# Optimization experiments

Hardware: AMD Instinct MI355X
Metric: run time of the kernel (lower is better)

Reference implementation:

```python
import jax, jax.numpy as jnp
import numpy as np

NUM_HEADS = 16  # matches init_kwargs


def _linear(x, W, b):
    # torch nn.Linear: x @ W.T + b
    return jnp.matmul(x, W.T) + b


def setup_inputs() -> dict:
    key = jax.random.key(0)
    ks = jax.random.split(key, 5)
    B, S, Dm = 8, 2048, 1024
    scale = 0.02
    return {
        "q": jax.random.normal(ks[0], (B, S, Dm), dtype=jnp.float32),
        "k": jax.random.normal(ks[1], (B, S, Dm), dtype=jnp.float32),
        "v": jax.random.normal(ks[2], (B, S, Dm), dtype=jnp.float32),
        "W": jax.random.normal(ks[3], (Dm, Dm), dtype=jnp.float32) * scale,
        "b": jax.random.normal(ks[4], (Dm,), dtype=jnp.float32) * scale,
    }


def reference(q, k, v, W, b):
    B, S, Dm = q.shape
    H = NUM_HEADS
    D = Dm // H  # head_dim

    def proj(x):
        # linear -> view(B, S, H, D) -> transpose(2, 3): (B, S, D, H)
        # NOTE: original code transposes dims 2 and 3 (head_dim <-> heads),
        # NOT the usual (1, 2); we reproduce that exactly.
        y = _linear(x, W, b).reshape(B, S, H, D)
        return jnp.swapaxes(y, 2, 3)  # (B, S, D, H)

    qh, kh, vh = proj(q), proj(k), proj(v)

    # scores: (B, S, D, H) @ (B, S, H, D) -> (B, S, D, D), scaled by sqrt(head_dim)
    logits = jnp.einsum("bsdh,bseh->bsde", qh, kh) / jnp.sqrt(jnp.float32(D))
    attn = jax.nn.softmax(logits, axis=-1)
    out = jnp.einsum("bsde,bseh->bsdh", attn, vh)  # (B, S, D, H)

    # transpose(1, 2) -> (B, D, S, H), then view(B, -1, model_dim)
    concat = jnp.swapaxes(out, 1, 2).reshape(B, -1, Dm)  # (B, S, Dm)
    return _linear(concat, W, b)
```

## Files before the change

kernel.cpp:

```cpp
#include <hip/hip_runtime.h>
#include <hip/hip_fp16.h>
#include <math.h>

typedef _Float16 f16;
typedef _Float16 half8_t __attribute__((ext_vector_type(8)));
typedef _Float16 half4_t __attribute__((ext_vector_type(4)));
typedef _Float16 half2_t __attribute__((ext_vector_type(2)));
typedef __fp16   fp16x2  __attribute__((ext_vector_type(2)));
typedef float    float4_t __attribute__((ext_vector_type(4)));

__device__ f16 Wh[1024 * 1024];
__device__ f16 Xh[3ul * 16777216];

__device__ __forceinline__ void gl_lds16(const void* g, void* l) {
    __builtin_amdgcn_global_load_lds(
        (const __attribute__((address_space(1))) void*)g,
        (__attribute__((address_space(3))) void*)l,
        16, 0, 0);
}

__device__ __forceinline__ half2_t pkrtz(float a, float b) {
    fp16x2 r = __builtin_amdgcn_cvt_pkrtz(a, b);
    return __builtin_bit_cast(half2_t, r);
}

__device__ __forceinline__ half8_t cvt8(float4_t lo, float4_t hi) {
    half2_t p0 = pkrtz(lo[0], lo[1]);
    half2_t p1 = pkrtz(lo[2], lo[3]);
    half2_t p2 = pkrtz(hi[0], hi[1]);
    half2_t p3 = pkrtz(hi[2], hi[3]);
    half8_t r;
    r[0] = p0[0]; r[1] = p0[1]; r[2] = p1[0]; r[3] = p1[1];
    r[4] = p2[0]; r[5] = p2[1]; r[6] = p3[0]; r[7] = p3[1];
    return r;
}

__global__ __launch_bounds__(256) void convert_w_kernel(const float* __restrict__ W) {
    const int i = (blockIdx.x * 256 + threadIdx.x) * 8;
    const float4_t a = *(const float4_t*)(W + i);
    const float4_t b = *(const float4_t*)(W + i + 4);
    half8_t h;
#pragma unroll
    for (int t = 0; t < 4; ++t) h[t] = (f16)a[t];
#pragma unroll
    for (int t = 0; t < 4; ++t) h[4 + t] = (f16)b[t];
    *(half8_t*)(Wh + i) = h;
}

__global__ __launch_bounds__(256) void convert_x_kernel(
    const float* __restrict__ q, const float* __restrict__ k,
    const float* __restrict__ v)
{
    const int z = blockIdx.z;
    const float* src = (z == 0) ? q : (z == 1) ? k : v;
    f16* dst = Xh + (size_t)z * 16777216;
    const size_t i = ((size_t)blockIdx.x * 256 + threadIdx.x) * 8;
    const float4_t a = *(const float4_t*)(src + i);
    const float4_t b = *(const float4_t*)(src + i + 4);
    *(half8_t*)(dst + i) = cvt8(a, b);
}


__device__ __forceinline__ void stage16(const f16* __restrict__ base, f16* dst,
                                        int tid, int kt) {
#pragma unroll
    for (int it = 0; it < 4; ++it) {
        const int ch = tid + it * 512;
        const int r = ch >> 3, s = ch & 7;
        gl_lds16(base + (size_t)r * 1024 + kt + ((s ^ (r & 7)) << 3), dst + ch * 8);
    }
}

template <typename TC>
__device__ __forceinline__ void gemm_tile256(const f16* __restrict__ A,
                                             const float* __restrict__ bias,
                                             TC* __restrict__ C,
                                             int row0, int col0) {
    constexpr int K = 1024, N = 1024, NT = 16;
    __shared__ __align__(16) f16 smem[65536];
    f16* const Asb = smem;
    f16* const Bsb = smem + 32768;

    const int tid  = threadIdx.x;
    const int lane = tid & 63;
    const int wave = tid >> 6;
    const int wr   = wave >> 2;
    const int wc   = wave & 3;
    const int lrow = lane & 15;
    const int kq   = lane >> 4;

    const f16* const Ag = A + (size_t)row0 * K;
    const f16* const Bg = Wh + (size_t)col0 * K;

    float4_t acc[8][4];
#pragma unroll
    for (int i = 0; i < 8; ++i)
#pragma unroll
        for (int j = 0; j < 4; ++j)
            acc[i][j] = (float4_t){0.f, 0.f, 0.f, 0.f};

    stage16(Ag, Asb, tid, 0);
    stage16(Bg, Bsb, tid, 0);

    for (int u = 0; u < NT; ++u) {
        const int cur = u & 1;
        const f16* const Ac = Asb + (cur << 14);
        const f16* const Bc = Bsb + (cur << 14);
        f16* const An = Asb + ((cur ^ 1) << 14);
        f16* const Bn = Bsb + ((cur ^ 1) << 14);
        const int kn = ((u + 1) & (NT - 1)) * 64;

        stage16(Ag, An, tid, kn);
        stage16(Bg, Bn, tid, kn);
        asm volatile("s_waitcnt vmcnt(8)" ::: "memory");
        __builtin_amdgcn_s_barrier();

        half8_t bfv[4][2];
#pragma unroll
        for (int j = 0; j < 4; ++j) {
            const int n = wc * 64 + j * 16 + lrow;
#pragma unroll
            for (int ks = 0; ks < 2; ++ks)
                bfv[j][ks] = *(const half8_t*)(Bc + n * 64 + (((ks * 4 + kq) ^ (n & 7)) << 3));
        }

        {
            half8_t afv[4][2];
#pragma unroll
            for (int i = 0; i < 4; ++i) {
                const int m = wr * 128 + i * 16 + lrow;
#pragma unroll
                for (int ks = 0; ks < 2; ++ks)
                    afv[i][ks] = *(const half8_t*)(Ac + m * 64 + (((ks * 4 + kq) ^ (m & 7)) << 3));
            }
            __builtin_amdgcn_s_setprio(1);
#pragma unroll
            for (int i = 0; i < 4; ++i)
#pragma unroll
                for (int j = 0; j < 4; ++j)
#pragma unroll
                    for (int ks = 0; ks < 2; ++ks)
                        acc[i][j] = __builtin_amdgcn_mfma_f32_16x16x32_f16(
                            afv[i][ks], bfv[j][ks], acc[i][j], 0, 0, 0);
            __builtin_amdgcn_s_setprio(0);
        }

        {
            half8_t afv[4][2];
#pragma unroll
            for (int i = 0; i < 4; ++i) {
                const int m = wr * 128 + (4 + i) * 16 + lrow;
#pragma unroll
                for (int ks = 0; ks < 2; ++ks)
                    afv[i][ks] = *(const half8_t*)(Ac + m * 64 + (((ks * 4 + kq) ^ (m & 7)) << 3));
            }
            __builtin_amdgcn_s_setprio(1);
#pragma unroll
            for (int i = 0; i < 4; ++i)
#pragma unroll
                for (int j = 0; j < 4; ++j)
#pragma unroll
                    for (int ks = 0; ks < 2; ++ks)
                        acc[4 + i][j] = __builtin_amdgcn_mfma_f32_16x16x32_f16(
                            afv[i][ks], bfv[j][ks], acc[4 + i][j], 0, 0, 0);
            __builtin_amdgcn_s_setprio(0);
        }

        asm volatile("s_waitcnt lgkmcnt(0)" ::: "memory");
        __builtin_amdgcn_s_barrier();
    }
    asm volatile("s_waitcnt vmcnt(0)" ::: "memory");

    const int ccol  = lane & 15;
    const int rbase = (lane >> 4) << 2;
#pragma unroll
    for (int j = 0; j < 4; ++j) {
        const int gcol = col0 + wc * 64 + j * 16 + ccol;
        const float bv = bias[gcol];
#pragma unroll
        for (int i = 0; i < 8; ++i) {
#pragma unroll
            for (int r = 0; r < 4; ++r) {
                const int grow = row0 + wr * 128 + i * 16 + rbase + r;
                C[(size_t)grow * N + gcol] = (TC)(acc[i][j][r] + bv);
            }
        }
    }
}

template <typename TC>
__global__ __launch_bounds__(512, 2) void gemm_kernel(
    const f16* __restrict__ A, const float* __restrict__ bias,
    TC* __restrict__ C) {
    const int f    = blockIdx.x + 64 * blockIdx.y;
    const int virt = (f & 7) * 32 + (f >> 3);
    gemm_tile256<TC>(A, bias, C, ((virt >> 2) & 63) * 256, (virt & 3) * 256);
}

__global__ __launch_bounds__(512, 2) void gemm_proj_kernel(
    const float* __restrict__ bias,
    f16* __restrict__ cq, f16* __restrict__ ck, f16* __restrict__ cv) {
    const int f    = blockIdx.x + 64 * (blockIdx.y + 4 * blockIdx.z);
    const int virt = (f & 7) * 96 + (f >> 3);
    const int y = virt & 3, x = (virt >> 2) & 63, z = virt >> 8;
    f16* C = (z == 0) ? cq : (z == 1) ? ck : cv;
    gemm_tile256<f16>(Xh + (size_t)z * 16777216, bias, C, x * 256, y * 256);
}

__global__ __launch_bounds__(256) void attn_kernel(
    const f16* __restrict__ pq, const f16* __restrict__ pk,
    const f16* __restrict__ pv, f16* __restrict__ outp)
{
    __shared__ __align__(16) f16 Qs[4][64][24];
    __shared__ __align__(16) f16 Ks[4][64][24];
    __shared__ __align__(16) f16 Vs[4][16][72];
    __shared__ __align__(16) f16 Os[4][64][24];
    const int lane = threadIdx.x & 63;
    const int wave = threadIdx.x >> 6;
    const int p0 = blockIdx.x * 4;
    const int p = p0 + wave;
    const f16* qptr = pq + (size_t)p * 1024;
    const f16* kptr = pk + (size_t)p * 1024;
    const f16* vptr = pv + (size_t)p * 1024;

    {
        const int h  = lane >> 2;
        const int c0 = (lane & 3) << 4;
        const half8_t q0 = *(const half8_t*)(qptr + lane * 16);
        const half8_t q1 = *(const half8_t*)(qptr + lane * 16 + 8);
        const half8_t k0 = *(const half8_t*)(kptr + lane * 16);
        const half8_t k1 = *(const half8_t*)(kptr + lane * 16 + 8);
#pragma unroll
        for (int t = 0; t < 8; ++t) {
            Qs[wave][c0 + t][h]     = q0[t];
            Qs[wave][c0 + 8 + t][h] = q1[t];
            Ks[wave][c0 + t][h]     = k0[t];
            Ks[wave][c0 + 8 + t][h] = k1[t];
        }
        const half8_t v0 = *(const half8_t*)(vptr + lane * 16);
        const half8_t v1 = *(const half8_t*)(vptr + lane * 16 + 8);
        *(half8_t*)&Vs[wave][h][c0]     = v0;
        *(half8_t*)&Vs[wave][h][c0 + 8] = v1;
    }
    __syncthreads();

    const int g  = lane >> 4;
    const int lc = lane & 15;

    half4_t ka[4], qb[4];
#pragma unroll
    for (int t = 0; t < 4; ++t) {
        ka[t] = *(const half4_t*)&Ks[wave][16 * t + lc][4 * g];
        qb[t] = *(const half4_t*)&Qs[wave][16 * t + lc][4 * g];
    }
    float4_t s[4][4];
#pragma unroll
    for (int et = 0; et < 4; ++et)
#pragma unroll
        for (int dt = 0; dt < 4; ++dt)
            s[et][dt] = __builtin_amdgcn_mfma_f32_16x16x16f16(
                ka[et], qb[dt], (float4_t){0.f, 0.f, 0.f, 0.f}, 0, 0, 0);

    float inv[4];
#pragma unroll
    for (int dt = 0; dt < 4; ++dt) {
        float m = s[0][dt][0];
#pragma unroll
        for (int et = 0; et < 4; ++et)
#pragma unroll
            for (int r = 0; r < 4; ++r) m = fmaxf(m, s[et][dt][r]);
        m = fmaxf(m, __shfl_xor(m, 16));
        m = fmaxf(m, __shfl_xor(m, 32));
        float sum = 0.f;
#pragma unroll
        for (int et = 0; et < 4; ++et)
#pragma unroll
            for (int r = 0; r < 4; ++r) {
                const float t = __expf((s[et][dt][r] - m) * 0.125f);
                s[et][dt][r] = t;
                sum += t;
            }
        sum += __shfl_xor(sum, 16);
        sum += __shfl_xor(sum, 32);
        inv[dt] = 1.f / sum;
    }

    half4_t pa[4][4];
#pragma unroll
    for (int kt = 0; kt < 4; ++kt)
#pragma unroll
        for (int dt = 0; dt < 4; ++dt) {
            const half2_t lo = pkrtz(s[kt][dt][0] * inv[dt], s[kt][dt][1] * inv[dt]);
            const half2_t hi = pkrtz(s[kt][dt][2] * inv[dt], s[kt][dt][3] * inv[dt]);
            half4_t f;
            f[0] = lo[0]; f[1] = lo[1]; f[2] = hi[0]; f[3] = hi[1];
            pa[kt][dt] = f;
        }

    float4_t o[4];
#pragma unroll
    for (int dt = 0; dt < 4; ++dt) o[dt] = (float4_t){0.f, 0.f, 0.f, 0.f};
#pragma unroll
    for (int kt = 0; kt < 4; ++kt) {
        const half4_t vb = *(const half4_t*)&Vs[wave][lc][16 * kt + 4 * g];
#pragma unroll
        for (int dt = 0; dt < 4; ++dt)
            o[dt] = __builtin_amdgcn_mfma_f32_16x16x16f16(pa[kt][dt], vb, o[dt], 0, 0, 0);
    }

#pragma unroll
    for (int dt = 0; dt < 4; ++dt)
#pragma unroll
        for (int r = 0; r < 4; ++r)
            Os[wave][16 * dt + 4 * g + r][lc] = (f16)o[dt][r];
    __syncthreads();

    const int b0 = p0 >> 11;
    const int s0 = p0 & 2047;
#pragma unroll
    for (int hf = 0; hf < 2; ++hf) {
        const int u  = threadIdx.x + hf * 256;
        const int d  = u >> 3;
        const int si = (u >> 1) & 3;
        const int uh = u & 1;
        const half8_t val = *(const half8_t*)&Os[si][d][uh * 8];
        f16* dst = outp + ((size_t)(b0 * 64 + d) * 2048 + (s0 + si)) * 16 + uh * 8;
        *(half8_t*)dst = val;
    }
}

extern "C" void kernel_launch(void* const* d_in, const int* in_sizes, int n_in,
                              void* d_out, int out_size, void* d_ws, size_t ws_size,
                              hipStream_t stream)
{
    const float* q    = (const float*)d_in[0];
    const float* k    = (const float*)d_in[1];
    const float* v    = (const float*)d_in[2];
    const float* W    = (const float*)d_in[3];
    const float* bias = (const float*)d_in[4];
    float* out = (float*)d_out;

    const int M = 16384;
    const size_t elems = (size_t)M * 1024;

    f16* projq = (f16*)d_ws;
    f16* attn  = projq + elems;
    f16* projk = (f16*)d_out;
    f16* projv = projk + elems;

    convert_w_kernel<<<512, 256, 0, stream>>>(W);
    dim3 gridc(8192, 1, 3);
    convert_x_kernel<<<gridc, 256, 0, stream>>>(q, k, v);

    dim3 gridp(M / 256, 1024 / 256, 3);
    gemm_proj_kernel<<<gridp, 512, 0, stream>>>(bias, projq, projk, projv);
    attn_kernel<<<M / 4, 256, 0, stream>>>(projq, projk, projv, attn);
    dim3 gridf(M / 256, 1024 / 256);
    gemm_kernel<float><<<gridf, 512, 0, stream>>>(attn, bias, out);
}
```

Before: 446.4 us.

## Interleave half-tile prefetches with MFMA quadrants and stage fp16 epilogue through LDS

Splits each K-step of the 256x256 GEMM into four MFMA quadrants and spreads half-sized global-to-LDS loads between them. The A tile is now prefetched two steps ahead into the buffer just consumed, and the B tile one step ahead. This gives finer-grained overlap of memory loads with compute, at the cost of more barriers per iteration. For fp16 outputs, the epilogue writes results to swizzled LDS and then stores coalesced 16-byte vectors to global memory instead of scattered 2-byte stores.

```diff
diff --git a/kernel.cpp b/kernel.cpp
--- a/kernel.cpp
+++ b/kernel.cpp
@@ -61,10 +61,10 @@
 }
 
 
-__device__ __forceinline__ void stage16(const f16* __restrict__ base, f16* dst,
-                                        int tid, int kt) {
-#pragma unroll
-    for (int it = 0; it < 4; ++it) {
+__device__ __forceinline__ void stage_half(const f16* __restrict__ base, f16* dst,
+                                           int tid, int kt, int half) {
+#pragma unroll
+    for (int it = 2 * half; it < 2 * half + 2; ++it) {
         const int ch = tid + it * 512;
         const int r = ch >> 3, s = ch & 7;
         gl_lds16(base + (size_t)r * 1024 + kt + ((s ^ (r & 7)) << 3), dst + ch * 8);
@@ -99,90 +99,153 @@
         for (int j = 0; j < 4; ++j)
             acc[i][j] = (float4_t){0.f, 0.f, 0.f, 0.f};
 
-    stage16(Ag, Asb, tid, 0);
-    stage16(Bg, Bsb, tid, 0);
+    stage_half(Ag, Asb, tid, 0, 0);
+    stage_half(Ag, Asb, tid, 0, 1);
+    stage_half(Bg, Bsb, tid, 0, 0);
+    stage_half(Bg, Bsb, tid, 0, 1);
+    stage_half(Ag, Asb + 16384, tid, 64, 0);
+    stage_half(Ag, Asb + 16384, tid, 64, 1);
 
     for (int u = 0; u < NT; ++u) {
-        const int cur = u & 1;
-        const f16* const Ac = Asb + (cur << 14);
-        const f16* const Bc = Bsb + (cur << 14);
-        f16* const An = Asb + ((cur ^ 1) << 14);
-        f16* const Bn = Bsb + ((cur ^ 1) << 14);
-        const int kn = ((u + 1) & (NT - 1)) * 64;
-
-        stage16(Ag, An, tid, kn);
-        stage16(Bg, Bn, tid, kn);
-        asm volatile("s_waitcnt vmcnt(8)" ::: "memory");
-        __builtin_amdgcn_s_barrier();
-
-        half8_t bfv[4][2];
-#pragma unroll
-        for (int j = 0; j < 4; ++j) {
+        const int c = u & 1;
+        const f16* const Ac = Asb + (c << 14);
+        const f16* const Bc = Bsb + (c << 14);
+        f16* const Bn = Bsb + ((c ^ 1) << 14);
+        f16* const Af = Asb + (c << 14);
+        const int k1 = ((u + 1) & (NT - 1)) * 64;
+        const int k2 = ((u + 2) & (NT - 1)) * 64;
+
+        half8_t afv[8][2], bfv[4][2];
+
+        stage_half(Bg, Bn, tid, k1, 0);
+        asm volatile("s_waitcnt vmcnt(6)" ::: "memory");
+        __builtin_amdgcn_s_barrier();
+#pragma unroll
+        for (int i = 0; i < 4; ++i) {
+            const int m = wr * 128 + i * 16 + lrow;
+#pragma unroll
+            for (int ks = 0; ks < 2; ++ks)
+                afv[i][ks] = *(const half8_t*)(Ac + m * 64 + (((ks * 4 + kq) ^ (m & 7)) << 3));
+        }
+#pragma unroll
+        for (int j = 0; j < 2; ++j) {
             const int n = wc * 64 + j * 16 + lrow;
 #pragma unroll
             for (int ks = 0; ks < 2; ++ks)
                 bfv[j][ks] = *(const half8_t*)(Bc + n * 64 + (((ks * 4 + kq) ^ (n & 7)) << 3));
         }
-
-        {
-            half8_t afv[4][2];
-#pragma unroll
-            for (int i = 0; i < 4; ++i) {
-                const int m = wr * 128 + i * 16 + lrow;
+        __builtin_amdgcn_s_setprio(1);
+#pragma unroll
+        for (int i = 0; i < 4; ++i)
+#pragma unroll
+            for (int j = 0; j < 2; ++j)
 #pragma unroll
                 for (int ks = 0; ks < 2; ++ks)
-                    afv[i][ks] = *(const half8_t*)(Ac + m * 64 + (((ks * 4 + kq) ^ (m & 7)) << 3));
-            }
-            __builtin_amdgcn_s_setprio(1);
-#pragma unroll
-            for (int i = 0; i < 4; ++i)
-#pragma unroll
-                for (int j = 0; j < 4; ++j)
-#pragma unroll
-                    for (int ks = 0; ks < 2; ++ks)
-                        acc[i][j] = __builtin_amdgcn_mfma_f32_16x16x32_f16(
-                            afv[i][ks], bfv[j][ks], acc[i][j], 0, 0, 0);
-            __builtin_amdgcn_s_setprio(0);
-        }
-
-        {
-            half8_t afv[4][2];
-#pragma unroll
-            for (int i = 0; i < 4; ++i) {
-                const int m = wr * 128 + (4 + i) * 16 + lrow;
+                    acc[i][j] = __builtin_amdgcn_mfma_f32_16x16x32_f16(
+                        afv[i][ks], bfv[j][ks], acc[i][j], 0, 0, 0);
+        __builtin_amdgcn_s_setprio(0);
+        __builtin_amdgcn_s_barrier();
+
+#pragma unroll
+        for (int i = 4; i < 8; ++i) {
+            const int m = wr * 128 + i * 16 + lrow;
+#pragma unroll
+            for (int ks = 0; ks < 2; ++ks)
+                afv[i][ks] = *(const half8_t*)(Ac + m * 64 + (((ks * 4 + kq) ^ (m & 7)) << 3));
+        }
+#pragma unroll
+        for (int j = 2; j < 4; ++j) {
+            const int n = wc * 64 + j * 16 + lrow;
+#pragma unroll
+            for (int ks = 0; ks < 2; ++ks)
+                bfv[j][ks] = *(const half8_t*)(Bc + n * 64 + (((ks * 4 + kq) ^ (n & 7)) << 3));
+        }
+        stage_half(Bg, Bn, tid, k1, 1);
+        __builtin_amdgcn_s_barrier();
+        __builtin_amdgcn_s_setprio(1);
+#pragma unroll
+        for (int i = 0; i < 4; ++i)
+#pragma unroll
+            for (int j = 2; j < 4; ++j)
 #pragma unroll
                 for (int ks = 0; ks < 2; ++ks)
-                    afv[i][ks] = *(const half8_t*)(Ac + m * 64 + (((ks * 4 + kq) ^ (m & 7)) << 3));
-            }
-            __builtin_amdgcn_s_setprio(1);
-#pragma unroll
-            for (int i = 0; i < 4; ++i)
-#pragma unroll
-                for (int j = 0; j < 4; ++j)
-#pragma unroll
-                    for (int ks = 0; ks < 2; ++ks)
-                        acc[4 + i][j] = __builtin_amdgcn_mfma_f32_16x16x32_f16(
-                            afv[i][ks], bfv[j][ks], acc[4 + i][j], 0, 0, 0);
-            __builtin_amdgcn_s_setprio(0);
-        }
-
+                    acc[i][j] = __builtin_amdgcn_mfma_f32_16x16x32_f16(
+                        afv[i][ks], bfv[j][ks], acc[i][j], 0, 0, 0);
+        __builtin_amdgcn_s_setprio(0);
         asm volatile("s_waitcnt lgkmcnt(0)" ::: "memory");
         __builtin_amdgcn_s_barrier();
+
+        stage_half(Ag, Af, tid, k2, 0);
+        __builtin_amdgcn_s_barrier();
+        __builtin_amdgcn_s_setprio(1);
+#pragma unroll
+        for (int i = 4; i < 8; ++i)
+#pragma unroll
+            for (int j = 0; j < 2; ++j)
+#pragma unroll
+                for (int ks = 0; ks < 2; ++ks)
+                    acc[i][j] = __builtin_amdgcn_mfma_f32_16x16x32_f16(
+                        afv[i][ks], bfv[j][ks], acc[i][j], 0, 0, 0);
+        __builtin_amdgcn_s_setprio(0);
+        __builtin_amdgcn_s_barrier();
+
+        stage_half(Ag, Af, tid, k2, 1);
+        __builtin_amdgcn_s_barrier();
+        __builtin_amdgcn_s_setprio(1);
+#pragma unroll
+        for (int i = 4; i < 8; ++i)
+#pragma unroll
+            for (int j = 2; j < 4; ++j)
+#pragma unroll
+                for (int ks = 0; ks < 2; ++ks)
+                    acc[i][j] = __builtin_amdgcn_mfma_f32_16x16x32_f16(
+                        afv[i][ks], bfv[j][ks], acc[i][j], 0, 0, 0);
+        __builtin_amdgcn_s_setprio(0);
+        __builtin_amdgcn_s_barrier();
     }
     asm volatile("s_waitcnt vmcnt(0)" ::: "memory");
+    __builtin_amdgcn_s_barrier();
 
     const int ccol  = lane & 15;
     const int rbase = (lane >> 4) << 2;
-#pragma unroll
-    for (int j = 0; j < 4; ++j) {
-        const int gcol = col0 + wc * 64 + j * 16 + ccol;
-        const float bv = bias[gcol];
-#pragma unroll
-        for (int i = 0; i < 8; ++i) {
-#pragma unroll
-            for (int r = 0; r < 4; ++r) {
-                const int grow = row0 + wr * 128 + i * 16 + rbase + r;
-                C[(size_t)grow * N + gcol] = (TC)(acc[i][j][r] + bv);
+
+    if constexpr (sizeof(TC) == 2) {
+        f16* const Cs = smem;
+#pragma unroll
+        for (int j = 0; j < 4; ++j) {
+            const int gcol = wc * 64 + j * 16 + ccol;
+            const float bv = bias[col0 + gcol];
+#pragma unroll
+            for (int i = 0; i < 8; ++i) {
+                const int grow = wr * 128 + i * 16 + rbase;
+                const int cx = gcol ^ (((grow >> 2) & 3) << 4);
+#pragma unroll
+                for (int r = 0; r < 4; ++r)
+                    Cs[(grow + r) * 256 + cx] = (f16)(acc[i][j][r] + bv);
+            }
+        }
+        __builtin_amdgcn_s_barrier();
+#pragma unroll
+        for (int p = 0; p < 16; ++p) {
+            const int idx = tid + p * 512;
+            const int row = idx >> 5;
+            const int col = (idx & 31) * 8;
+            const int cx  = col ^ (((row >> 2) & 3) << 4);
+            const half8_t v = *(const half8_t*)(Cs + row * 256 + cx);
+            *(half8_t*)((TC*)C + (size_t)(row0 + row) * N + col0 + col) = v;
+        }
+    } else {
+#pragma unroll
+        for (int j = 0; j < 4; ++j) {
+            const int gcol = col0 + wc * 64 + j * 16 + ccol;
+            const float bv = bias[gcol];
+#pragma unroll
+            for (int i = 0; i < 8; ++i) {
+#pragma unroll
+                for (int r = 0; r < 4; ++r) {
+                    const int grow = row0 + wr * 128 + i * 16 + rbase + r;
+                    C[(size_t)grow * N + gcol] = (TC)(acc[i][j][r] + bv);
+                }
             }
         }
     }
```

Result: faster. 415.6 us (-6.9%).
